# Optimization experiments

Measured on AMD Instinct MI355X. Metric: run time of the kernel, lower is better.

The kernel has to match this reference:

```python
import math
import jax, jax.numpy as jnp
import numpy as np

DIM = 256
GROUPS = 32
EPS = 1e-5


def setup_inputs() -> dict:
    key = jax.random.key(0)
    ks = jax.random.split(key, 6)
    b, c, h, w = 4, DIM, 64, 64
    x = jax.random.normal(ks[0], (b, c, h, w), dtype=jnp.float32)
    norm_scale = jnp.ones((c,), dtype=jnp.float32)
    norm_bias = jnp.zeros((c,), dtype=jnp.float32)
    w_qkv = jax.random.normal(ks[1], (3 * c, c), dtype=jnp.float32) / math.sqrt(c)
    w_proj = jax.random.normal(ks[2], (c, c), dtype=jnp.float32) / math.sqrt(c)
    b_proj = jnp.zeros((c,), dtype=jnp.float32)
    return {"x": x, "norm_scale": norm_scale, "norm_bias": norm_bias,
            "w_qkv": w_qkv, "w_proj": w_proj, "b_proj": b_proj}


def _group_norm(x, scale, bias):
    b, c, h, w = x.shape
    xg = x.reshape(b, GROUPS, c // GROUPS, h, w)
    mean = jnp.mean(xg, axis=(2, 3, 4), keepdims=True)
    var = jnp.var(xg, axis=(2, 3, 4), keepdims=True)
    xn = ((xg - mean) * jax.lax.rsqrt(var + EPS)).reshape(b, c, h, w)
    return xn * scale[None, :, None, None] + bias[None, :, None, None]


def reference(x, norm_scale, norm_bias, w_qkv, w_proj, b_proj):
    b, c, h, w = x.shape
    n = h * w
    xn = _group_norm(x, norm_scale, norm_bias)          # residual uses normalized x (as in source)
    xf = xn.reshape(b, c, n)                            # (b, c, n)
    qkv = jnp.einsum('oc,bcn->bon', w_qkv, xf)          # 1x1 conv == channel matmul
    q, k, v = jnp.split(qkv, 3, axis=1)                 # each (b, c, n)
    attn = jnp.einsum('bci,bcj->bij', q, k) / math.sqrt(c)
    attn = jax.nn.softmax(attn, axis=-1)                # (b, n, n)
    out = jnp.einsum('bij,bcj->bci', attn, v)           # (b, c, n)
    out = jnp.einsum('oc,bcn->bon', w_proj, out) + b_proj[None, :, None]
    return out.reshape(b, c, h, w) + xn
```

## Files before the change

kernel.cpp:

```cpp
#include <hip/hip_runtime.h>
#include <hip/hip_fp8.h>
#include <cstdint>
#include <cstddef>

typedef __bf16 bf16;
typedef __attribute__((ext_vector_type(8))) __bf16 bf16x8;
typedef __attribute__((ext_vector_type(4))) float f32x4;
typedef __attribute__((ext_vector_type(4))) unsigned short u16x4;
typedef __attribute__((ext_vector_type(8))) unsigned short u16x8;

#define DEV __device__ __forceinline__

DEV unsigned short f2bf(float f) {
    unsigned int u = __builtin_bit_cast(unsigned int, f);
    u += 0x7FFFu + ((u >> 16) & 1u);
    return (unsigned short)(u >> 16);
}

DEV float bf2f(unsigned short h) {
    unsigned int u = ((unsigned int)h) << 16;
    return __builtin_bit_cast(float, u);
}

DEV unsigned char f2e4m3(float f) {
    __hip_fp8_e4m3 t(f);
    return (unsigned char)t.__x;
}

DEV void gload16(const void* g, void* l) {
    __builtin_amdgcn_global_load_lds(
        (const __attribute__((address_space(1))) unsigned int*)g,
        (__attribute__((address_space(3))) unsigned int*)l, 16, 0, 0);
}

DEV f32x4 mfma16(bf16x8 a, bf16x8 b, f32x4 c) {
    return __builtin_amdgcn_mfma_f32_16x16x32_bf16(a, b, c, 0, 0, 0);
}

__global__ __launch_bounds__(256) void k_pre(const float* __restrict__ wqkv,
        const float* __restrict__ wproj, const float* __restrict__ x,
        unsigned short* __restrict__ wq, unsigned short* __restrict__ wp,
        float* __restrict__ stats) {
    if (blockIdx.x < 1024) {
        int i = blockIdx.x * 256 + threadIdx.x;
        if (i < 768 * 256) {
            float v = wqkv[i];
            if (i < 512 * 256) v *= 0.3002806f;
            wq[i] = f2bf(v);
        } else {
            int j = i - 768 * 256;
            wp[j] = f2bf(wproj[j]);
        }
        return;
    }
    int bg = blockIdx.x - 1024;
    const float4* xp = (const float4*)(x + (size_t)bg * 32768);
    int t = threadIdx.x;
    float s = 0.f, sq = 0.f;
    #pragma unroll 4
    for (int i = 0; i < 32; ++i) {
        float4 v = xp[t + i * 256];
        s  += v.x + v.y + v.z + v.w;
        sq += v.x * v.x + v.y * v.y + v.z * v.z + v.w * v.w;
    }
    #pragma unroll
    for (int m = 1; m < 64; m <<= 1) { s += __shfl_xor(s, m); sq += __shfl_xor(sq, m); }
    __shared__ float red[8];
    int w = t >> 6;
    if ((t & 63) == 0) { red[w] = s; red[4 + w] = sq; }
    __syncthreads();
    if (t == 0) {
        s  = red[0] + red[1] + red[2] + red[3];
        sq = red[4] + red[5] + red[6] + red[7];
        float mean = s * (1.f / 32768.f);
        float var  = sq * (1.f / 32768.f) - mean * mean;
        stats[bg * 2]     = mean;
        stats[bg * 2 + 1] = rsqrtf(var + 1e-5f);
    }
}

__global__ __launch_bounds__(256) void k_gnapply(const float* __restrict__ x,
        const float* __restrict__ scale, const float* __restrict__ bias,
        const float* __restrict__ stats, unsigned short* __restrict__ xnT) {
    __shared__ __align__(16) unsigned short tsm[64][72];
    int t = threadIdx.x;
    int nb = blockIdx.x * 64, cb = blockIdx.y * 64, b = blockIdx.z;
    int cl = t >> 2, nc = (t & 3) * 16;
    int cg = cb + cl;
    float mean = stats[(b * 32 + (cg >> 3)) * 2];
    float rstd = stats[(b * 32 + (cg >> 3)) * 2 + 1];
    float sc = scale[cg] * rstd;
    float bi = bias[cg] - mean * sc;
    const float4* xrow = (const float4*)(x + ((size_t)(b * 256 + cg)) * 4096 + nb + nc);
    #pragma unroll
    for (int j = 0; j < 4; ++j) {
        float4 v = xrow[j];
        u16x4 us;
        us[0] = f2bf(v.x * sc + bi); us[1] = f2bf(v.y * sc + bi);
        us[2] = f2bf(v.z * sc + bi); us[3] = f2bf(v.w * sc + bi);
        *(u16x4*)&tsm[cl][nc + j * 4] = us;
    }
    __syncthreads();
    int nl = t >> 2, cc = (t & 3) * 16;
    u16x8 o0, o1;
    #pragma unroll
    for (int j = 0; j < 8; ++j) { o0[j] = tsm[cc + j][nl]; o1[j] = tsm[cc + 8 + j][nl]; }
    unsigned short* dst = xnT + ((size_t)(b * 4096 + nb + nl)) * 256 + cb + cc;
    *(u16x8*)dst = o0;
    *(u16x8*)(dst + 8) = o1;
}

__global__ __launch_bounds__(256) void k_qkv(const unsigned short* __restrict__ xnT,
        const unsigned short* __restrict__ wq, unsigned char* __restrict__ qk8,
        unsigned short* __restrict__ vT) {
    __shared__ __align__(16) char smem[75776];
    char* Asm = smem;
    char* Bsm = smem + 32768;
    unsigned short (*tsm)[72] = (unsigned short (*)[72])(smem + 65536);
    int t = threadIdx.x, l = t & 63, w = t >> 6;
    int mb = blockIdx.x * 64;
    int nb0 = blockIdx.y * 128;
    #pragma unroll
    for (int i = 0; i < 8; ++i) {
        int idx = (w * 8 + i) * 64 + l;
        int r = idx >> 5, p = idx & 31;
        gload16(xnT + (size_t)(mb + r) * 256 + ((p ^ (r & 7)) * 8), Asm + (w * 8 + i) * 1024);
    }
    #pragma unroll
    for (int i = 0; i < 8; ++i) {
        int idx = (w * 8 + i) * 64 + l;
        int r = idx >> 5, p = idx & 31;
        gload16(wq + (size_t)(nb0 + r) * 256 + ((p ^ (r & 7)) * 8), Bsm + (w * 8 + i) * 1024);
    }
    __syncthreads();
    int arow = w * 16 + (l & 15);
    bf16x8 af[8];
    #pragma unroll
    for (int ks = 0; ks < 8; ++ks)
        af[ks] = *(const bf16x8*)(Asm + arow * 512 + (((ks * 4 + (l >> 4)) ^ (arow & 7)) << 4));
    int row0 = mb + w * 16 + (l >> 4) * 4;

    #pragma unroll
    for (int half = 0; half < 2; ++half) {
        int nb = nb0 + half * 64;
        f32x4 acc[4];
        #pragma unroll
        for (int i = 0; i < 4; ++i) acc[i] = f32x4{0.f, 0.f, 0.f, 0.f};
        #pragma unroll
        for (int sub = 0; sub < 4; ++sub) {
            int brow = sub * 16 + (l & 15);
            #pragma unroll
            for (int ks = 0; ks < 8; ++ks) {
                bf16x8 bb = *(const bf16x8*)(Bsm + brow * 512 + (((ks * 4 + (l >> 4)) ^ (brow & 7)) << 4));
                acc[sub] = mfma16(af[ks], bb, acc[sub]);
            }
        }
        if (nb < 512) {
            #pragma unroll
            for (int sub = 0; sub < 4; ++sub) {
                #pragma unroll
                for (int r = 0; r < 4; ++r)
                    qk8[(size_t)(row0 + r) * 512 + nb + sub * 16 + (l & 15)] = f2e4m3(acc[sub][r]);
            }
        } else {
            int rt = w * 16 + (l >> 4) * 4;
            #pragma unroll
            for (int sub = 0; sub < 4; ++sub) {
                int ct = sub * 16 + (l & 15);
                #pragma unroll
                for (int r = 0; r < 4; ++r)
                    tsm[rt + r][ct] = f2bf(acc[sub][r]);
            }
            __syncthreads();
            int clc = t >> 2, nn = (t & 3) * 16;
            u16x8 o0, o1;
            #pragma unroll
            for (int j = 0; j < 8; ++j) { o0[j] = tsm[nn + j][clc]; o1[j] = tsm[nn + 8 + j][clc]; }
            int b = mb >> 12;
            int nloc = mb & 4095;
            unsigned short* dst = vT + (size_t)(b * 256 + (nb - 512) + clc) * 4096 + nloc + nn;
            *(u16x8*)dst = o0;
            *(u16x8*)(dst + 8) = o1;
        }
        if (half == 0) {
            __syncthreads();
            #pragma unroll
            for (int i = 0; i < 8; ++i) {
                int idx = (w * 8 + i) * 64 + l;
                int r = idx >> 5, p = idx & 31;
                gload16(wq + (size_t)(nb0 + 64 + r) * 256 + ((p ^ (r & 7)) * 8), Bsm + (w * 8 + i) * 1024);
            }
            __syncthreads();
        }
    }
}

struct AttnState {
    f32x4 acc[16];
    f32x4 accSum;
    float m_run[4];
};

DEV void attn_compute(const char* Ksm, const char* Vsm, char* Psm,
                      const long long qf8[8], AttnState& st, int l) {
    f32x4 s[4];
    __builtin_amdgcn_s_setprio(1);
    #pragma unroll
    for (int jt = 0; jt < 4; ++jt) {
        f32x4 a = f32x4{0.f, 0.f, 0.f, 0.f};
        int jr = jt * 16 + (l & 15);
        #pragma unroll
        for (int ks = 0; ks < 8; ++ks) {
            int c8 = ks * 4 + (l >> 4);
            long long kb = *(const long long*)(Ksm + jr * 256 +
                            (((c8 >> 1) ^ (jr & 7)) << 4) + (c8 & 1) * 8);
            a = __builtin_amdgcn_mfma_f32_16x16x32_fp8_fp8(qf8[ks], kb, a, 0, 0, 0);
        }
        s[jt] = a;
    }
    __builtin_amdgcn_s_setprio(0);

    float tm[4];
    #pragma unroll
    for (int r = 0; r < 4; ++r) {
        float v = fmaxf(fmaxf(s[0][r], s[1][r]), fmaxf(s[2][r], s[3][r]));
        #pragma unroll
        for (int mm = 1; mm < 16; mm <<= 1) v = fmaxf(v, __shfl_xor(v, mm));
        tm[r] = v;
    }
    int defer = 1;
    #pragma unroll
    for (int r = 0; r < 4; ++r) defer &= (tm[r] <= st.m_run[r] + 8.f) ? 1 : 0;
    bool alldef = __all(defer);
    if (!alldef) {
        float sf[4];
        #pragma unroll
        for (int r = 0; r < 4; ++r) {
            float mn = fmaxf(st.m_run[r], tm[r]);
            sf[r] = __builtin_amdgcn_exp2f(st.m_run[r] - mn);
            st.m_run[r] = mn;
        }
        #pragma unroll
        for (int i = 0; i < 16; ++i) {
            st.acc[i][0] *= sf[0]; st.acc[i][1] *= sf[1];
            st.acc[i][2] *= sf[2]; st.acc[i][3] *= sf[3];
        }
        st.accSum[0] *= sf[0]; st.accSum[1] *= sf[1];
        st.accSum[2] *= sf[2]; st.accSum[3] *= sf[3];
    }

    #pragma unroll
    for (int jt = 0; jt < 4; ++jt) {
        #pragma unroll
        for (int r = 0; r < 4; ++r) {
            float pv = __builtin_amdgcn_exp2f(s[jt][r] - st.m_run[r]);
            int row = (l >> 4) * 4 + r;
            int j = jt * 16 + (l & 15);
            int byteoff = row * 128 + (((j >> 3) ^ (row & 7)) << 4) + (j & 7) * 2;
            *(unsigned short*)(Psm + byteoff) = f2bf(pv);
        }
    }
    asm volatile("s_waitcnt lgkmcnt(0)" ::: "memory");
    __builtin_amdgcn_sched_barrier(0);

    bf16x8 onesv;
    #pragma unroll
    for (int j = 0; j < 8; ++j) onesv[j] = (__bf16)1.0f;
    __builtin_amdgcn_s_setprio(1);
    #pragma unroll
    for (int js = 0; js < 2; ++js) {
        int pr = l & 15;
        bf16x8 pa = *(const bf16x8*)(Psm + pr * 128 + (((js * 4 + (l >> 4)) ^ (pr & 7)) << 4));
        #pragma unroll
        for (int sub = 0; sub < 16; ++sub) {
            int cr = sub * 16 + (l & 15);
            bf16x8 vb = *(const bf16x8*)(Vsm + cr * 128 + (((js * 4 + (l >> 4)) ^ (cr & 7)) << 4));
            st.acc[sub] = mfma16(pa, vb, st.acc[sub]);
        }
        st.accSum = mfma16(pa, onesv, st.accSum);
    }
    __builtin_amdgcn_s_setprio(0);
}

#define ATTN_STAGE(KN, VN, kvn)                                                   \
    do {                                                                          \
        _Pragma("unroll")                                                         \
        for (int i_ = 0; i_ < 2; ++i_) {              \
            int e_ = (w * 2 + i_) * 64 + l;                                       \
            int r_ = e_ >> 4, p_ = e_ & 15;                                       \
            gload16(kg8 + (size_t)((kvn) + r_) * 512 + ((p_ ^ (r_ & 7)) * 16),    \
                    (KN) + (w * 2 + i_) * 1024);                                  \
        }                                                                         \
        _Pragma("unroll")                                                         \
        for (int i_ = 0; i_ < 4; ++i_) {                        \
            int e_ = (w * 4 + i_) * 64 + l;                                       \
            int r_ = e_ >> 3, p_ = e_ & 7;                                        \
            gload16(vg0 + (size_t)r_ * 4096 + (kvn) + ((p_ ^ (r_ & 7)) * 8),      \
                    (VN) + (w * 4 + i_) * 1024);                                  \
        }                                                                         \
    } while (0)

__global__ __launch_bounds__(512, 2) void k_attn(const unsigned char* __restrict__ qk8,
        const unsigned short* __restrict__ vT, unsigned short* __restrict__ Opart,
        float* __restrict__ ml) {
    __shared__ __align__(16) char smem[114688];
    char* Ksm0 = smem;
    char* Vsm0 = smem + 16384;
    char* Ksm1 = smem + 49152;
    char* Vsm1 = smem + 65536;
    int t = threadIdx.x, l = t & 63, w = t >> 6;
    char* Psm = smem + 98304 + w * 2048;
    int bid = blockIdx.x;
    int combo = bid & 7;
    int b = combo >> 1;
    int half = combo & 1;
    int qb = (bid >> 3) * 128;
    int kv0 = half * 2048;

    const unsigned char* qrow8 = qk8 + (size_t)(b * 4096 + qb + w * 16 + (l & 15)) * 512;
    long long qf8[8];
    #pragma unroll
    for (int ks = 0; ks < 8; ++ks)
        qf8[ks] = *(const long long*)(qrow8 + ks * 32 + (l >> 4) * 8);

    AttnState st;
    #pragma unroll
    for (int i = 0; i < 16; ++i) st.acc[i] = f32x4{0.f, 0.f, 0.f, 0.f};
    st.accSum = f32x4{0.f, 0.f, 0.f, 0.f};
    #pragma unroll
    for (int r = 0; r < 4; ++r) st.m_run[r] = -3.0e38f;

    const unsigned char* kg8 = qk8 + (size_t)(b * 4096) * 512 + 256;
    const unsigned short* vg0 = vT + (size_t)(b * 256) * 4096;

    ATTN_STAGE(Ksm0, Vsm0, kv0);
    __syncthreads();

    for (int kv = kv0; kv < kv0 + 2048; kv += 128) {
        ATTN_STAGE(Ksm1, Vsm1, kv + 64);
        attn_compute(Ksm0, Vsm0, Psm, qf8, st, l);
        __syncthreads();
        int kvn2 = (kv + 128 < kv0 + 2048) ? (kv + 128) : kv0;
        ATTN_STAGE(Ksm0, Vsm0, kvn2);
        attn_compute(Ksm1, Vsm1, Psm, qf8, st, l);
        __syncthreads();
    }

    float inv[4];
    #pragma unroll
    for (int r = 0; r < 4; ++r) inv[r] = 1.f / st.accSum[r];
    unsigned short* orow = Opart + (size_t)half * 16384 * 256 +
                           (size_t)(b * 4096 + qb + w * 16) * 256;
    #pragma unroll
    for (int sub = 0; sub < 16; ++sub) {
        #pragma unroll
        for (int r = 0; r < 4; ++r)
            orow[(size_t)((l >> 4) * 4 + r) * 256 + sub * 16 + (l & 15)] = f2bf(st.acc[sub][r] * inv[r]);
    }
    if ((l & 15) == 0) {
        size_t mlbase = (size_t)(b * 4096 + qb + w * 16 + (l >> 4) * 4) * 4;
        #pragma unroll
        for (int r = 0; r < 4; ++r) {
            ml[mlbase + (size_t)r * 4 + half * 2]     = st.m_run[r];
            ml[mlbase + (size_t)r * 4 + half * 2 + 1] = st.accSum[r];
        }
    }
}

__global__ __launch_bounds__(256) void k_proj(const unsigned short* __restrict__ Opart,
        const float* __restrict__ ml, const unsigned short* __restrict__ wp,
        const float* __restrict__ bproj, const float* __restrict__ x,
        const float* __restrict__ nscale, const float* __restrict__ nbias,
        const float* __restrict__ stats, float* __restrict__ out) {
    __shared__ __align__(16) char smem[65536];
    char* Asm = smem;
    char* Bsm = smem + 32768;
    int t = threadIdx.x, l = t & 63, w = t >> 6;
    int mb = blockIdx.x * 64, nb = blockIdx.y * 64;
    #pragma unroll
    for (int i = 0; i < 8; ++i) {
        int idx = (w * 8 + i) * 64 + l;
        int r = idx >> 5, p = idx & 31;
        size_t grow = (size_t)(mb + r);
        const u16x8* o1p = (const u16x8*)(Opart + grow * 256 + ((p ^ (r & 7)) * 8));
        const u16x8* o2p = (const u16x8*)((const unsigned short*)o1p + (size_t)16384 * 256);
        float m1 = ml[grow * 4],     l1 = ml[grow * 4 + 1];
        float m2 = ml[grow * 4 + 2], l2 = ml[grow * 4 + 3];
        float m = fmaxf(m1, m2);
        float a1 = __builtin_amdgcn_exp2f(m1 - m) * l1;
        float a2 = __builtin_amdgcn_exp2f(m2 - m) * l2;
        float zinv = 1.f / (a1 + a2);
        float w1 = a1 * zinv, w2 = a2 * zinv;
        u16x8 o1 = *o1p, o2 = *o2p, a;
        #pragma unroll
        for (int j = 0; j < 8; ++j) a[j] = f2bf(w1 * bf2f(o1[j]) + w2 * bf2f(o2[j]));
        *(u16x8*)(Asm + (w * 8 + i) * 1024 + l * 16) = a;
    }
    #pragma unroll
    for (int i = 0; i < 8; ++i) {
        int idx = (w * 8 + i) * 64 + l;
        int r = idx >> 5, p = idx & 31;
        gload16(wp + (size_t)(nb + r) * 256 + ((p ^ (r & 7)) * 8), Bsm + (w * 8 + i) * 1024);
    }
    __syncthreads();
    int arow = w * 16 + (l & 15);
    bf16x8 af[8];
    #pragma unroll
    for (int ks = 0; ks < 8; ++ks)
        af[ks] = *(const bf16x8*)(Asm + arow * 512 + (((ks * 4 + (l >> 4)) ^ (arow & 7)) << 4));
    f32x4 acc[4];
    #pragma unroll
    for (int i = 0; i < 4; ++i) acc[i] = f32x4{0.f, 0.f, 0.f, 0.f};
    #pragma unroll
    for (int sub = 0; sub < 4; ++sub) {
        int brow = sub * 16 + (l & 15);
        #pragma unroll
        for (int ks = 0; ks < 8; ++ks) {
            bf16x8 bb = *(const bf16x8*)(Bsm + brow * 512 + (((ks * 4 + (l >> 4)) ^ (brow & 7)) << 4));
            acc[sub] = mfma16(af[ks], bb, acc[sub]);
        }
    }
    __syncthreads();
    float* tr = (float*)smem;
    #pragma unroll
    for (int sub = 0; sub < 4; ++sub) {
        int o = sub * 16 + (l & 15);
        *(f32x4*)(tr + o * 68 + w * 16 + (l >> 4) * 4) = acc[sub];
    }
    __syncthreads();
    int b = mb >> 12;
    int nloc = mb & 4095;
    #pragma unroll
    for (int it = 0; it < 4; ++it) {
        int e = it * 256 + t;
        int o = e >> 4, m4 = (e & 15) * 4;
        f32x4 v = *(const f32x4*)(tr + o * 68 + m4);
        int c = nb + o;
        float bv = bproj[c];
        float mean = stats[(b * 32 + (c >> 3)) * 2];
        float rstd = stats[(b * 32 + (c >> 3)) * 2 + 1];
        float sc = nscale[c] * rstd;
        float bi = nbias[c] - mean * sc;
        size_t off = ((size_t)(b * 256 + c)) * 4096 + nloc + m4;
        float4 xx = *(const float4*)(x + off);
        float4 ov;
        ov.x = v[0] + bv + (xx.x * sc + bi);
        ov.y = v[1] + bv + (xx.y * sc + bi);
        ov.z = v[2] + bv + (xx.z * sc + bi);
        ov.w = v[3] + bv + (xx.w * sc + bi);
        *(float4*)(out + off) = ov;
    }
}

extern "C" void kernel_launch(void* const* d_in, const int* in_sizes, int n_in,
                              void* d_out, int out_size, void* d_ws, size_t ws_size,
                              hipStream_t stream) {
    const float* x      = (const float*)d_in[0];
    const float* nscale = (const float*)d_in[1];
    const float* nbias  = (const float*)d_in[2];
    const float* wqkv   = (const float*)d_in[3];
    const float* wproj  = (const float*)d_in[4];
    const float* bproj  = (const float*)d_in[5];
    float* out = (float*)d_out;

    char* ws = (char*)d_ws;
    float* stats = (float*)ws;
    unsigned short* xnT = (unsigned short*)(ws + 4096);
    unsigned short* wq  = xnT + 4194304;
    unsigned short* wp  = wq + 768 * 256;
    unsigned short* vT  = wp + 256 * 256;
    float* ml = (float*)(vT + (size_t)4 * 256 * 4096);
    unsigned char* qk8 = (unsigned char*)(ml + 65536);
    unsigned short* Opart = (unsigned short*)(qk8 + (size_t)16384 * 512);

    hipLaunchKernelGGL(k_pre,     dim3(1152),       dim3(256), 0, stream, wqkv, wproj, x, wq, wp, stats);
    hipLaunchKernelGGL(k_gnapply, dim3(64, 4, 4),   dim3(256), 0, stream, x, nscale, nbias, stats, xnT);
    hipLaunchKernelGGL(k_qkv,     dim3(256, 6),     dim3(256), 0, stream, xnT, wq, qk8, vT);
    hipLaunchKernelGGL(k_attn,    dim3(256),        dim3(512), 0, stream, qk8, vT, Opart, ml);
    hipLaunchKernelGGL(k_proj,    dim3(256, 4),     dim3(256), 0, stream, Opart, ml, wp, bproj, x, nscale, nbias, stats, out);
}
```

Before: 132.9 us.

## Store V and softmax probabilities as FP8 and use FP8 MFMA for PV

The QKV kernel now writes the transposed V tensor as e4m3 bytes instead of bf16. The attention kernel stores P in FP8 and computes P·V and the row sums with fp8 MFMAs, with new swizzled LDS layouts for V and P. This halves V global traffic and LDS footprint (shared memory drops from 112KB to 72KB) and doubles MFMA throughput for the PV product. In exchange, precision drops for both probabilities and V values, which could affect accuracy tolerance.

```diff
diff --git a/kernel.cpp b/kernel.cpp
--- a/kernel.cpp
+++ b/kernel.cpp
@@ -8,6 +8,8 @@
 typedef __attribute__((ext_vector_type(4))) float f32x4;
 typedef __attribute__((ext_vector_type(4))) unsigned short u16x4;
 typedef __attribute__((ext_vector_type(8))) unsigned short u16x8;
+typedef __attribute__((ext_vector_type(16))) unsigned char u8x16;
+typedef __attribute__((ext_vector_type(2))) long long llx2;
 
 #define DEV __device__ __forceinline__
 
@@ -35,6 +37,10 @@
 
 DEV f32x4 mfma16(bf16x8 a, bf16x8 b, f32x4 c) {
     return __builtin_amdgcn_mfma_f32_16x16x32_bf16(a, b, c, 0, 0, 0);
+}
+
+DEV f32x4 mfma8(long long a, long long b, f32x4 c) {
+    return __builtin_amdgcn_mfma_f32_16x16x32_fp8_fp8(a, b, c, 0, 0, 0);
 }
 
 __global__ __launch_bounds__(256) void k_pre(const float* __restrict__ wqkv,
@@ -112,7 +118,7 @@
 
 __global__ __launch_bounds__(256) void k_qkv(const unsigned short* __restrict__ xnT,
         const unsigned short* __restrict__ wq, unsigned char* __restrict__ qk8,
-        unsigned short* __restrict__ vT) {
+        unsigned char* __restrict__ vT8) {
     __shared__ __align__(16) char smem[75776];
     char* Asm = smem;
     char* Bsm = smem + 32768;
@@ -172,15 +178,18 @@
                     tsm[rt + r][ct] = f2bf(acc[sub][r]);
             }
             __syncthreads();
-            int clc = t >> 2, nn = (t & 3) * 16;
-            u16x8 o0, o1;
+            int clc = t >> 2, g = t & 3;
+            u8x16 ob;
             #pragma unroll
-            for (int j = 0; j < 8; ++j) { o0[j] = tsm[nn + j][clc]; o1[j] = tsm[nn + 8 + j][clc]; }
+            for (int j = 0; j < 8; ++j) {
+                ob[j]     = f2e4m3(bf2f(tsm[g * 8 + j][clc]));
+                ob[8 + j] = f2e4m3(bf2f(tsm[32 + g * 8 + j][clc]));
+            }
             int b = mb >> 12;
             int nloc = mb & 4095;
-            unsigned short* dst = vT + (size_t)(b * 256 + (nb - 512) + clc) * 4096 + nloc + nn;
-            *(u16x8*)dst = o0;
-            *(u16x8*)(dst + 8) = o1;
+            int d = (nb - 512) + clc;
+            unsigned char* dst = vT8 + ((size_t)(b * 256 + d)) * 4096 + nloc + g * 16;
+            *(u8x16*)dst = ob;
         }
         if (half == 0) {
             __syncthreads();
@@ -214,7 +223,7 @@
             int c8 = ks * 4 + (l >> 4);
             long long kb = *(const long long*)(Ksm + jr * 256 +
                             (((c8 >> 1) ^ (jr & 7)) << 4) + (c8 & 1) * 8);
-            a = __builtin_amdgcn_mfma_f32_16x16x32_fp8_fp8(qf8[ks], kb, a, 0, 0, 0);
+            a = mfma8(qf8[ks], kb, a);
         }
         s[jt] = a;
     }
@@ -256,28 +265,31 @@
             float pv = __builtin_amdgcn_exp2f(s[jt][r] - st.m_run[r]);
             int row = (l >> 4) * 4 + r;
             int j = jt * 16 + (l & 15);
-            int byteoff = row * 128 + (((j >> 3) ^ (row & 7)) << 4) + (j & 7) * 2;
-            *(unsigned short*)(Psm + byteoff) = f2bf(pv);
+            int g = (j >> 3) & 3, js = j >> 5;
+            int bo = row * 64 + (((g ^ ((row >> 1) & 3))) << 4) + js * 8 + (j & 7);
+            *(unsigned char*)(Psm + bo) = f2e4m3(pv);
         }
     }
     asm volatile("s_waitcnt lgkmcnt(0)" ::: "memory");
     __builtin_amdgcn_sched_barrier(0);
 
-    bf16x8 onesv;
-    #pragma unroll
-    for (int j = 0; j < 8; ++j) onesv[j] = (__bf16)1.0f;
+    const long long ones8 = 0x3838383838383838LL;
     __builtin_amdgcn_s_setprio(1);
-    #pragma unroll
-    for (int js = 0; js < 2; ++js) {
+    {
         int pr = l & 15;
-        bf16x8 pa = *(const bf16x8*)(Psm + pr * 128 + (((js * 4 + (l >> 4)) ^ (pr & 7)) << 4));
+        llx2 pa01 = *(const llx2*)(Psm + pr * 64 +
+                     ((((l >> 4)) ^ ((pr >> 1) & 3)) << 4));
         #pragma unroll
         for (int sub = 0; sub < 16; ++sub) {
-            int cr = sub * 16 + (l & 15);
-            bf16x8 vb = *(const bf16x8*)(Vsm + cr * 128 + (((js * 4 + (l >> 4)) ^ (cr & 7)) << 4));
-            st.acc[sub] = mfma16(pa, vb, st.acc[sub]);
-        }
-        st.accSum = mfma16(pa, onesv, st.accSum);
+            int d = sub * 16 + (l & 15);
+            int dp = d >> 1, h = d & 1;
+            llx2 vb01 = *(const llx2*)(Vsm + dp * 128 +
+                         ((h * 4 + ((l >> 4) ^ (dp & 3))) << 4));
+            st.acc[sub] = mfma8(pa01[0], vb01[0], st.acc[sub]);
+            st.acc[sub] = mfma8(pa01[1], vb01[1], st.acc[sub]);
+        }
+        st.accSum = mfma8(pa01[0], ones8, st.accSum);
+        st.accSum = mfma8(pa01[1], ones8, st.accSum);
     }
     __builtin_amdgcn_s_setprio(0);
 }
@@ -292,24 +304,25 @@
                     (KN) + (w * 2 + i_) * 1024);                                  \
         }                                                                         \
         _Pragma("unroll")                                                         \
-        for (int i_ = 0; i_ < 4; ++i_) {                        \
-            int e_ = (w * 4 + i_) * 64 + l;                                       \
-            int r_ = e_ >> 3, p_ = e_ & 7;                                        \
-            gload16(vg0 + (size_t)r_ * 4096 + (kvn) + ((p_ ^ (r_ & 7)) * 8),      \
-                    (VN) + (w * 4 + i_) * 1024);                                  \
+        for (int i_ = 0; i_ < 2; ++i_) {          \
+            int e_ = (w * 2 + i_) * 64 + l;                                       \
+            int dp_ = e_ >> 3, c_ = e_ & 7;                                       \
+            int h_ = c_ >> 2, g_ = (c_ & 3) ^ (dp_ & 3);                          \
+            gload16(vg8 + (size_t)(2 * dp_ + h_) * 4096 + (kvn) + g_ * 16,        \
+                    (VN) + (w * 2 + i_) * 1024);                                  \
         }                                                                         \
     } while (0)
 
 __global__ __launch_bounds__(512, 2) void k_attn(const unsigned char* __restrict__ qk8,
-        const unsigned short* __restrict__ vT, unsigned short* __restrict__ Opart,
+        const unsigned char* __restrict__ vT8, unsigned short* __restrict__ Opart,
         float* __restrict__ ml) {
-    __shared__ __align__(16) char smem[114688];
+    __shared__ __align__(16) char smem[73728];
     char* Ksm0 = smem;
     char* Vsm0 = smem + 16384;
-    char* Ksm1 = smem + 49152;
-    char* Vsm1 = smem + 65536;
+    char* Ksm1 = smem + 32768;
+    char* Vsm1 = smem + 49152;
     int t = threadIdx.x, l = t & 63, w = t >> 6;
-    char* Psm = smem + 98304 + w * 2048;
+    char* Psm = smem + 65536 + w * 1024;
     int bid = blockIdx.x;
     int combo = bid & 7;
     int b = combo >> 1;
@@ -331,7 +344,7 @@
     for (int r = 0; r < 4; ++r) st.m_run[r] = -3.0e38f;
 
     const unsigned char* kg8 = qk8 + (size_t)(b * 4096) * 512 + 256;
-    const unsigned short* vg0 = vT + (size_t)(b * 256) * 4096;
+    const unsigned char* vg8 = vT8 + (size_t)(b * 256) * 4096;
 
     ATTN_STAGE(Ksm0, Vsm0, kv0);
     __syncthreads();
@@ -468,14 +481,14 @@
     unsigned short* xnT = (unsigned short*)(ws + 4096);
     unsigned short* wq  = xnT + 4194304;
     unsigned short* wp  = wq + 768 * 256;
-    unsigned short* vT  = wp + 256 * 256;
-    float* ml = (float*)(vT + (size_t)4 * 256 * 4096);
+    unsigned char* vT8  = (unsigned char*)(wp + 256 * 256);
+    float* ml = (float*)(vT8 + (size_t)4 * 256 * 4096);
     unsigned char* qk8 = (unsigned char*)(ml + 65536);
     unsigned short* Opart = (unsigned short*)(qk8 + (size_t)16384 * 512);
 
     hipLaunchKernelGGL(k_pre,     dim3(1152),       dim3(256), 0, stream, wqkv, wproj, x, wq, wp, stats);
     hipLaunchKernelGGL(k_gnapply, dim3(64, 4, 4),   dim3(256), 0, stream, x, nscale, nbias, stats, xnT);
-    hipLaunchKernelGGL(k_qkv,     dim3(256, 6),     dim3(256), 0, stream, xnT, wq, qk8, vT);
-    hipLaunchKernelGGL(k_attn,    dim3(256),        dim3(512), 0, stream, qk8, vT, Opart, ml);
+    hipLaunchKernelGGL(k_qkv,     dim3(256, 6),     dim3(256), 0, stream, xnT, wq, qk8, vT8);
+    hipLaunchKernelGGL(k_attn,    dim3(256),        dim3(512), 0, stream, qk8, vT8, Opart, ml);
     hipLaunchKernelGGL(k_proj,    dim3(256, 4),     dim3(256), 0, stream, Opart, ml, wp, bproj, x, nscale, nbias, stats, out);
 }
```

Result: faster. 129.1 us, median of 2 (-2.9%).
